# Optimization experiments

Hardware: AMD Instinct MI355X
Metric: run time of the kernel (lower is better)

## Reference

```python
import jax, jax.numpy as jnp
import numpy as np

B, T, D, H = 8, 1024, 512, 8
HD = D // H  # per-head hidden = embed_dim // n_head = 64
EPS = 1e-5


def setup_inputs() -> dict:
    key = jax.random.key(0)
    ks = jax.random.split(key, 8)
    x = jax.random.normal(ks[0], (B, T, D), dtype=jnp.float32)
    sc = 1.0 / np.sqrt(D)
    Wq = jax.random.normal(ks[1], (D, H * HD), dtype=jnp.float32) * sc
    Wk = jax.random.normal(ks[2], (D, H * HD), dtype=jnp.float32) * sc
    Wp = jax.random.normal(ks[3], (H * HD, D), dtype=jnp.float32) * sc
    bq = jnp.zeros((H * HD,), jnp.float32)
    bk = jnp.zeros((H * HD,), jnp.float32)
    bp = jnp.zeros((D,), jnp.float32)
    w_mlp = jax.random.normal(ks[4], (2 * HD,), dtype=jnp.float32) * 0.1
    ln_g = jnp.ones((D,), jnp.float32)
    ln_b = jnp.zeros((D,), jnp.float32)
    return {"x": x, "Wq": Wq, "bq": bq, "Wk": Wk, "bk": bk,
            "Wp": Wp, "bp": bp, "w_mlp": w_mlp, "ln_g": ln_g, "ln_b": ln_b}


def reference(x, Wq, bq, Wk, bk, Wp, bp, w_mlp, ln_g, ln_b):
    b, t, d = x.shape
    h, hd = H, HD
    # q/k projections, split into heads: [B,T,H,hd]
    qx = (x @ Wq + bq).reshape(b, t, h, hd)
    kx = (x @ Wk + bk).reshape(b, t, h, hd)
    # MLP score: tanh(concat(k_j, q_i) . w) == tanh(k_j.w[:hd] + q_i.w[hd:])
    k_s = jnp.einsum('bkhd,d->bkh', kx, w_mlp[:hd])   # [B,K,H]
    q_s = jnp.einsum('bqhd,d->bqh', qx, w_mlp[hd:])   # [B,Q,H]
    score = jnp.tanh(q_s[:, :, None, :] + k_s[:, None, :, :])  # [B,Q,K,H]
    attn = jax.nn.softmax(score, axis=2)  # softmax over k_len
    # values are the key projection kx (bmm(score, kx) in original)
    out = jnp.einsum('bqkh,bkhd->bqhd', attn, kx).reshape(b, t, h * hd)
    out = out @ Wp + bp  # output projection (dropout is identity at eval)
    # residual + LayerNorm
    y = x + out
    mu = jnp.mean(y, axis=-1, keepdims=True)
    var = jnp.var(y, axis=-1, keepdims=True)
    yn = (y - mu) * jax.lax.rsqrt(var + EPS)
    return yn * ln_g + ln_b
```

## Files before the change

### kernel.cpp

```cpp
#include <hip/hip_runtime.h>
#include <cstddef>

#define TT 1024
#define DDIM 512
#define HH 8
#define NND 128
#define NW 72

typedef __attribute__((ext_vector_type(8))) short bfrag;
typedef __attribute__((ext_vector_type(4))) float facc;

#define SC2   2.8853900817779268f
#define L2E   1.4426950408889634f

static __device__ __forceinline__ unsigned bfrne(float f) {
    unsigned u = __float_as_uint(f);
    return (u + 0x7fffu + ((u >> 16) & 1u)) >> 16;
}
static __device__ __forceinline__ unsigned pack2rne(float a, float b) {
    return bfrne(a) | (bfrne(b) << 16);
}
static __device__ __forceinline__ unsigned pack2hu(float a, float b) {
    return ((__float_as_uint(a) + 0x8000u) >> 16) |
           ((__float_as_uint(b) + 0x8000u) & 0xffff0000u);
}
static __device__ __forceinline__ void gl2lds16(const void* g, void* l) {
    __builtin_amdgcn_global_load_lds(
        (const __attribute__((address_space(1))) unsigned int*)g,
        (__attribute__((address_space(3))) unsigned int*)l, 16, 0, 0);
}
static __device__ __forceinline__ float wfun(float z2) {
    float t = __builtin_amdgcn_exp2f(z2);
    float r = __builtin_amdgcn_rcpf(t + 1.f);
    return __builtin_amdgcn_exp2f(fmaf(r, -2.f * L2E, L2E));
}

__global__ __launch_bounds__(256) void prepare_kernel(
    const float* __restrict__ x, const float* __restrict__ Wk,
    const float* __restrict__ Wp, const float* __restrict__ Wq,
    const float* __restrict__ bq, const float* __restrict__ wm,
    unsigned short* __restrict__ xb, unsigned short* __restrict__ WkT,
    unsigned short* __restrict__ WpT, unsigned short* __restrict__ vq2b,
    float* __restrict__ qsb2)
{
    const int bx = blockIdx.x, tid = threadIdx.x;
    if (bx < 2048) {
        const int lane = tid & 63, wave = tid >> 6;
        const int row = bx * 4 + wave;
        const float4* xr = (const float4*)(x + (size_t)row * DDIM);
        float4 x0 = xr[lane * 2], x1 = xr[lane * 2 + 1];
        uint4 st;
        st.x = pack2rne(x0.x, x0.y); st.y = pack2rne(x0.z, x0.w);
        st.z = pack2rne(x1.x, x1.y); st.w = pack2rne(x1.z, x1.w);
        int p = lane ^ (row & 7);
        *(uint4*)(xb + (size_t)row * DDIM + p * 8) = st;
    } else if (bx < 2176) {
        int idx = bx - 2048;
        const float* src = (idx & 64) ? Wp : Wk;
        unsigned short* dst = (idx & 64) ? WpT : WkT;
        idx &= 63;
        const int n0 = (idx & 7) * 64, k0 = (idx >> 3) * 64;
        __shared__ float sT[64][65];
        #pragma unroll
        for (int it = 0; it < 4; ++it) {
            int task = it * 256 + tid;
            int kr = task >> 4, c4 = (task & 15) * 4;
            float4 v = *(const float4*)(src + (size_t)(k0 + kr) * DDIM + n0 + c4);
            sT[kr][c4] = v.x; sT[kr][c4 + 1] = v.y; sT[kr][c4 + 2] = v.z; sT[kr][c4 + 3] = v.w;
        }
        __syncthreads();
        #pragma unroll
        for (int it = 0; it < 2; ++it) {
            int task = it * 256 + tid;
            int n = task >> 3, kg = task & 7;
            unsigned u[4];
            #pragma unroll
            for (int jj = 0; jj < 4; ++jj)
                u[jj] = pack2rne(sT[kg * 8 + jj * 2][n], sT[kg * 8 + jj * 2 + 1][n]);
            int p = ((k0 >> 3) + kg) ^ (n & 7);
            uint4 st; st.x = u[0]; st.y = u[1]; st.z = u[2]; st.w = u[3];
            *(uint4*)(dst + (size_t)(n0 + n) * DDIM + p * 8) = st;
        }
    } else {
        int idx = (bx - 2176) * 256 + tid;
        int h = idx >> 9, d = idx & 511;
        float s = 0.f;
        #pragma unroll 8
        for (int j = 0; j < 64; ++j)
            s = fmaf(Wq[(size_t)d * DDIM + h * 64 + j], wm[64 + j], s);
        vq2b[h * DDIM + d] = (unsigned short)bfrne(s * SC2);
        if (idx < HH) {
            float sb = 0.f;
            for (int j = 0; j < 64; ++j)
                sb = fmaf(bq[idx * 64 + j], wm[64 + j], sb);
            qsb2[idx] = sb * SC2;
        }
    }
}

__global__ __launch_bounds__(256) void gemm1_kernel(
    const unsigned short* __restrict__ A, const unsigned short* __restrict__ B,
    const float* __restrict__ bias, unsigned short* __restrict__ kxTg,
    float* __restrict__ ks2, const float* __restrict__ wm,
    const unsigned short* __restrict__ vq2b, const float* __restrict__ qsb2,
    float* __restrict__ qs2)
{
    __shared__ __align__(16) unsigned short smem[12288];
    unsigned short* sA = smem;
    unsigned short* sB = smem + 8192;
    const int tid = threadIdx.x, lane = tid & 63, wave = tid >> 6;
    const int l15 = lane & 15, quad = lane >> 4;
    const int h = blockIdx.x, row0 = blockIdx.y * 128;
    const int col0 = h * 64;

    facc acc[2][4]; facc accq[2];
    #pragma unroll
    for (int i = 0; i < 2; ++i) {
        #pragma unroll
        for (int j = 0; j < 4; ++j) { acc[i][j][0]=0.f; acc[i][j][1]=0.f; acc[i][j][2]=0.f; acc[i][j][3]=0.f; }
        accq[i][0]=0.f; accq[i][1]=0.f; accq[i][2]=0.f; accq[i][3]=0.f;
    }

    for (int k0 = 0; k0 < 512; k0 += 64) {
        #pragma unroll
        for (int it = 0; it < 4; ++it) {
            int g = it * 256 + tid;
            int r = g >> 3, kg = g & 7;
            gl2lds16(A + (size_t)(row0 + r) * 512 + k0 + kg * 8, &sA[g * 8]);
        }
        #pragma unroll
        for (int it = 0; it < 2; ++it) {
            int g = it * 256 + tid;
            int r = g >> 3, kg = g & 7;
            gl2lds16(B + (size_t)(col0 + r) * 512 + k0 + kg * 8, &sB[g * 8]);
        }
        __syncthreads();
        #pragma unroll
        for (int ks_ = 0; ks_ < 2; ++ks_) {
            int slot = (ks_ * 4 + quad) ^ (l15 & 7);
            bfrag a[2], b[4];
            #pragma unroll
            for (int i = 0; i < 2; ++i)
                a[i] = *(const bfrag*)&sA[(wave * 32 + i * 16 + l15) * 64 + slot * 8];
            #pragma unroll
            for (int nt = 0; nt < 4; ++nt)
                b[nt] = *(const bfrag*)&sB[(nt * 16 + l15) * 64 + slot * 8];
            bfrag bvq = *(const bfrag*)(vq2b + h * 512 + k0 + ks_ * 32 + quad * 8);
            #pragma unroll
            for (int i = 0; i < 2; ++i) {
                #pragma unroll
                for (int nt = 0; nt < 4; ++nt)
                    acc[i][nt] = __builtin_amdgcn_mfma_f32_16x16x32_bf16(a[i], b[nt], acc[i][nt], 0, 0, 0);
                accq[i] = __builtin_amdgcn_mfma_f32_16x16x32_bf16(a[i], bvq, accq[i], 0, 0, 0);
            }
        }
        __syncthreads();
    }

    const int bb = row0 >> 10, t0 = row0 & 1023;
    const float qsbh = qsb2[h];
    float bvv[4], wmv[4];
    #pragma unroll
    for (int nt = 0; nt < 4; ++nt) {
        bvv[nt] = bias[col0 + nt * 16 + l15];
        wmv[nt] = wm[nt * 16 + l15] * SC2;
    }
    float part[2][4];
    #pragma unroll
    for (int i = 0; i < 2; ++i)
        #pragma unroll
        for (int r = 0; r < 4; ++r) part[i][r] = 0.f;

    unsigned short* eT = smem;
    #pragma unroll
    for (int i = 0; i < 2; ++i) {
        int tr = wave * 32 + i * 16 + quad * 4;
        #pragma unroll
        for (int nt = 0; nt < 4; ++nt) {
            int col = nt * 16 + l15;
            float v0 = acc[i][nt][0] + bvv[nt], v1 = acc[i][nt][1] + bvv[nt];
            float v2 = acc[i][nt][2] + bvv[nt], v3 = acc[i][nt][3] + bvv[nt];
            part[i][0] = fmaf(wmv[nt], v0, part[i][0]);
            part[i][1] = fmaf(wmv[nt], v1, part[i][1]);
            part[i][2] = fmaf(wmv[nt], v2, part[i][2]);
            part[i][3] = fmaf(wmv[nt], v3, part[i][3]);
            *(unsigned*)&eT[col * 136 + tr]     = pack2rne(v0, v1);
            *(unsigned*)&eT[col * 136 + tr + 2] = pack2rne(v2, v3);
        }
    }
    #pragma unroll
    for (int i = 0; i < 2; ++i)
        #pragma unroll
        for (int r = 0; r < 4; ++r) {
            float p = part[i][r];
            p += __shfl_xor(p, 1); p += __shfl_xor(p, 2);
            p += __shfl_xor(p, 4); p += __shfl_xor(p, 8);
            if (l15 == 0) {
                size_t o = (size_t)(bb * HH + h) * TT + t0 + wave * 32 + i * 16 + quad * 4 + r;
                ks2[o] = p;
                qs2[o] = accq[i][r] + qsbh;
            }
        }
    __syncthreads();
    unsigned short* kxbase = kxTg + ((size_t)(bb * HH + h) * 64) * TT;
    #pragma unroll
    for (int it = 0; it < 4; ++it) {
        int task = it * 256 + tid;
        int col = task >> 4, seg = task & 15;
        uint4 v = *(const uint4*)&eT[col * 136 + seg * 8];
        int g = (t0 >> 3) + seg;
        int p = g ^ (col & 7);
        *(uint4*)(kxbase + (size_t)col * TT + p * 8) = v;
    }
}

__global__ __launch_bounds__(256) void attn_nodes_kernel(
    const unsigned short* __restrict__ kxTg, const float* __restrict__ qs2,
    const float* __restrict__ ks2, float* __restrict__ node_out,
    float* __restrict__ mn2, float* __restrict__ inv127)
{
    __shared__ __align__(16) unsigned short kxT[64 * 256];
    __shared__ float ksc[1024];
    __shared__ float redl[8];
    const int bh = blockIdx.x;
    const int tid = threadIdx.x, lane = tid & 63, wave = tid >> 6;
    const int l15 = lane & 15, quad = lane >> 4;

    ((float4*)ksc)[tid] = ((const float4*)(ks2 + (size_t)bh * TT))[tid];
    float4 q4 = ((const float4*)(qs2 + (size_t)bh * TT))[tid];
    float mn = fminf(fminf(q4.x, q4.y), fminf(q4.z, q4.w));
    float mx = fmaxf(fmaxf(q4.x, q4.y), fmaxf(q4.z, q4.w));
    #pragma unroll
    for (int off = 32; off > 0; off >>= 1) {
        mn = fminf(mn, __shfl_xor(mn, off));
        mx = fmaxf(mx, __shfl_xor(mx, off));
    }
    if (lane == 0) { redl[wave] = mn; redl[4 + wave] = mx; }
    __syncthreads();
    const float mnv = fminf(fminf(redl[0], redl[1]), fminf(redl[2], redl[3]));
    const float mxv = fmaxf(fmaxf(redl[4], redl[5]), fmaxf(redl[6], redl[7]));
    if (tid == 0) {
        mn2[bh] = mnv;
        inv127[bh] = 127.f / fmaxf(mxv - mnv, 1e-12f);
    }
    const float h2v = (mxv - mnv) * (1.f / 127.f);
    const float zA = mnv + (wave * 16 + l15) * h2v;
    const float zB = zA + 64.f * h2v;

    const unsigned short* kxbase = kxTg + (size_t)bh * 64 * TT;
    facc acc[2][4]; facc accZ[2];
    #pragma unroll
    for (int g = 0; g < 2; ++g) {
        #pragma unroll
        for (int i = 0; i < 4; ++i) { acc[g][i][0]=0.f; acc[g][i][1]=0.f; acc[g][i][2]=0.f; acc[g][i][3]=0.f; }
        accZ[g][0]=0.f; accZ[g][1]=0.f; accZ[g][2]=0.f; accZ[g][3]=0.f;
    }
    bfrag ones;
    #pragma unroll
    for (int j = 0; j < 8; ++j) ones[j] = (short)0x3F80;

    for (int ck = 0; ck < 4; ++ck) {
        #pragma unroll
        for (int it = 0; it < 8; ++it) {
            int g = it * 256 + tid;
            int d = g >> 5, j = g & 31;
            gl2lds16(kxbase + (size_t)d * TT + ck * 256 + j * 8, &kxT[g * 8]);
        }
        __syncthreads();
        #pragma unroll
        for (int kst = 0; kst < 8; ++kst) {
            const float* kvp = &ksc[ck * 256 + kst * 32 + quad * 8];
            float4 kv0 = *(const float4*)kvp;
            float4 kv1 = *(const float4*)(kvp + 4);
            int slot = (kst * 4 + quad) ^ (l15 & 7);
            bfrag bf_[4];
            #pragma unroll
            for (int dt = 0; dt < 4; ++dt)
                bf_[dt] = *(const bfrag*)&kxT[(dt * 16 + l15) * 256 + slot * 8];
            #pragma unroll
            for (int g = 0; g < 2; ++g) {
                float z = g ? zB : zA;
                union { unsigned u[4]; bfrag f; } afu;
                afu.u[0] = pack2hu(wfun(z + kv0.x), wfun(z + kv0.y));
                afu.u[1] = pack2hu(wfun(z + kv0.z), wfun(z + kv0.w));
                afu.u[2] = pack2hu(wfun(z + kv1.x), wfun(z + kv1.y));
                afu.u[3] = pack2hu(wfun(z + kv1.z), wfun(z + kv1.w));
                #pragma unroll
                for (int dt = 0; dt < 4; ++dt)
                    acc[g][dt] = __builtin_amdgcn_mfma_f32_16x16x32_bf16(afu.f, bf_[dt], acc[g][dt], 0, 0, 0);
                accZ[g] = __builtin_amdgcn_mfma_f32_16x16x32_bf16(afu.f, ones, accZ[g], 0, 0, 0);
            }
        }
        __syncthreads();
    }
    float* ob = node_out + (size_t)bh * NND * NW;
    #pragma unroll
    for (int g = 0; g < 2; ++g) {
        #pragma unroll
        for (int r = 0; r < 4; ++r) {
            int node = g * 64 + wave * 16 + quad * 4 + r;
            #pragma unroll
            for (int dt = 0; dt < 4; ++dt)
                ob[(size_t)node * NW + dt * 16 + l15] = acc[g][dt][r];
            if (l15 == 0) ob[(size_t)node * NW + 64] = accZ[g][r];
        }
    }
}

__global__ __launch_bounds__(256) void interp_kernel(
    const float* __restrict__ qs2, const float* __restrict__ node_out,
    const float* __restrict__ mn2, const float* __restrict__ inv127,
    unsigned short* __restrict__ attb)
{
    const int tid = threadIdx.x, lane = tid & 63, wave = tid >> 6;
    const int row = blockIdx.x * 4 + wave;
    const int b = row >> 10, t = row & 1023;
    const int hh2 = lane >> 5, dp = lane & 31;
    #pragma unroll
    for (int h0 = 0; h0 < 8; h0 += 2) {
        const int hh = h0 + hh2;
        const int bh = b * HH + hh;
        float qv = qs2[(size_t)bh * TT + t];
        float u = (qv - mn2[bh]) * inv127[bh];
        int i = (int)floorf(u) - 1;
        i = i < 0 ? 0 : (i > NND - 4 ? NND - 4 : i);
        float s = u - (float)i;
        float s1 = s - 1.f, s2 = s - 2.f, s3 = s - 3.f;
        float w0 = -s1 * s2 * s3 * (1.f / 6.f);
        float w1 = s * s2 * s3 * 0.5f;
        float w2 = -s * s1 * s3 * 0.5f;
        float w3 = s * s1 * s2 * (1.f / 6.f);
        const float* base = node_out + ((size_t)bh * NND + i) * NW;
        float2 v0 = *(const float2*)(base + 2 * dp);
        float2 v1 = *(const float2*)(base + NW + 2 * dp);
        float2 v2 = *(const float2*)(base + 2 * NW + 2 * dp);
        float2 v3 = *(const float2*)(base + 3 * NW + 2 * dp);
        float nx = w0 * v0.x + w1 * v1.x + w2 * v2.x + w3 * v3.x;
        float ny = w0 * v0.y + w1 * v1.y + w2 * v2.y + w3 * v3.y;
        float zz = w0 * base[64] + w1 * base[NW + 64] + w2 * base[2 * NW + 64] + w3 * base[3 * NW + 64];
        float rz = __builtin_amdgcn_rcpf(zz);
        unsigned pk = pack2rne(nx * rz, ny * rz);
        int col = hh * 64 + 2 * dp;
        int p = (col >> 3) ^ (row & 7);
        *(unsigned*)&attb[(size_t)row * DDIM + p * 8 + (col & 7)] = pk;
    }
}

__global__ __launch_bounds__(256) void gemm2_kernel(
    const unsigned short* __restrict__ A, const unsigned short* __restrict__ B,
    const float* __restrict__ bias, const float* __restrict__ x,
    unsigned short* __restrict__ yb)
{
    __shared__ __align__(16) unsigned short smem[12288];
    unsigned short* sA = smem;
    unsigned short* sB = smem + 8192;
    const int tid = threadIdx.x, lane = tid & 63, wave = tid >> 6;
    const int l15 = lane & 15, quad = lane >> 4;
    const int col0 = blockIdx.x * 64, row0 = blockIdx.y * 128;

    facc acc[2][4];
    #pragma unroll
    for (int i = 0; i < 2; ++i)
        #pragma unroll
        for (int j = 0; j < 4; ++j) { acc[i][j][0]=0.f; acc[i][j][1]=0.f; acc[i][j][2]=0.f; acc[i][j][3]=0.f; }

    for (int k0 = 0; k0 < 512; k0 += 64) {
        #pragma unroll
        for (int it = 0; it < 4; ++it) {
            int g = it * 256 + tid;
            int r = g >> 3, kg = g & 7;
            gl2lds16(A + (size_t)(row0 + r) * 512 + k0 + kg * 8, &sA[g * 8]);
        }
        #pragma unroll
        for (int it = 0; it < 2; ++it) {
            int g = it * 256 + tid;
            int r = g >> 3, kg = g & 7;
            gl2lds16(B + (size_t)(col0 + r) * 512 + k0 + kg * 8, &sB[g * 8]);
        }
        __syncthreads();
        #pragma unroll
        for (int ks_ = 0; ks_ < 2; ++ks_) {
            int slot = (ks_ * 4 + quad) ^ (l15 & 7);
            bfrag a[2], b[4];
            #pragma unroll
            for (int i = 0; i < 2; ++i)
                a[i] = *(const bfrag*)&sA[(wave * 32 + i * 16 + l15) * 64 + slot * 8];
            #pragma unroll
            for (int nt = 0; nt < 4; ++nt)
                b[nt] = *(const bfrag*)&sB[(nt * 16 + l15) * 64 + slot * 8];
            #pragma unroll
            for (int i = 0; i < 2; ++i)
                #pragma unroll
                for (int nt = 0; nt < 4; ++nt)
                    acc[i][nt] = __builtin_amdgcn_mfma_f32_16x16x32_bf16(a[i], b[nt], acc[i][nt], 0, 0, 0);
        }
        __syncthreads();
    }
    float bvv[4];
    #pragma unroll
    for (int nt = 0; nt < 4; ++nt) bvv[nt] = bias[col0 + nt * 16 + l15];
    unsigned short* yT = smem;
    #pragma unroll
    for (int i = 0; i < 2; ++i) {
        #pragma unroll
        for (int nt = 0; nt < 4; ++nt) {
            int col = nt * 16 + l15;
            #pragma unroll
            for (int r = 0; r < 4; ++r) {
                int row = wave * 32 + i * 16 + quad * 4 + r;
                float xv = x[(size_t)(row0 + row) * DDIM + col0 + col];
                float y = acc[i][nt][r] + bvv[nt] + xv;
                yT[row * 72 + col] = (unsigned short)bfrne(y);
            }
        }
    }
    __syncthreads();
    #pragma unroll
    for (int it = 0; it < 4; ++it) {
        int task = it * 256 + tid;
        int row = task >> 3, seg = task & 7;
        uint4 v = *(const uint4*)&yT[row * 72 + seg * 8];
        *(uint4*)(yb + (size_t)(row0 + row) * DDIM + col0 + seg * 8) = v;
    }
}

__global__ __launch_bounds__(256) void ln_kernel(
    const unsigned short* __restrict__ yb, const float* __restrict__ g,
    const float* __restrict__ bet, float* __restrict__ out)
{
    const int tid = threadIdx.x, lane = tid & 63, wave = tid >> 6;
    const int row = blockIdx.x * 4 + wave;
    uint4 v = *(const uint4*)(yb + (size_t)row * DDIM + lane * 8);
    float y[8];
    y[0] = __uint_as_float(v.x << 16); y[1] = __uint_as_float(v.x & 0xffff0000u);
    y[2] = __uint_as_float(v.y << 16); y[3] = __uint_as_float(v.y & 0xffff0000u);
    y[4] = __uint_as_float(v.z << 16); y[5] = __uint_as_float(v.z & 0xffff0000u);
    y[6] = __uint_as_float(v.w << 16); y[7] = __uint_as_float(v.w & 0xffff0000u);
    float s = 0.f, s2 = 0.f;
    #pragma unroll
    for (int i = 0; i < 8; ++i) { s += y[i]; s2 = fmaf(y[i], y[i], s2); }
    #pragma unroll
    for (int off = 32; off > 0; off >>= 1) {
        s += __shfl_xor(s, off);
        s2 += __shfl_xor(s2, off);
    }
    float mu = s * (1.f / 512.f);
    float var = s2 * (1.f / 512.f) - mu * mu;
    float inv = rsqrtf(var + 1e-5f);
    const float4* gp = (const float4*)(g + lane * 8);
    const float4* bp = (const float4*)(bet + lane * 8);
    float4 g0 = gp[0], g1 = gp[1], b0 = bp[0], b1 = bp[1];
    float4 o0, o1;
    o0.x = (y[0] - mu) * inv * g0.x + b0.x; o0.y = (y[1] - mu) * inv * g0.y + b0.y;
    o0.z = (y[2] - mu) * inv * g0.z + b0.z; o0.w = (y[3] - mu) * inv * g0.w + b0.w;
    o1.x = (y[4] - mu) * inv * g1.x + b1.x; o1.y = (y[5] - mu) * inv * g1.y + b1.y;
    o1.z = (y[6] - mu) * inv * g1.z + b1.z; o1.w = (y[7] - mu) * inv * g1.w + b1.w;
    float4* op = (float4*)(out + (size_t)row * DDIM);
    op[lane * 2] = o0; op[lane * 2 + 1] = o1;
}

extern "C" void kernel_launch(void* const* d_in, const int* in_sizes, int n_in,
                              void* d_out, int out_size, void* d_ws, size_t ws_size,
                              hipStream_t stream)
{
    const float* x    = (const float*)d_in[0];
    const float* Wq   = (const float*)d_in[1];
    const float* bq   = (const float*)d_in[2];
    const float* Wk   = (const float*)d_in[3];
    const float* bk   = (const float*)d_in[4];
    const float* Wp   = (const float*)d_in[5];
    const float* bp   = (const float*)d_in[6];
    const float* wm   = (const float*)d_in[7];
    const float* ln_g = (const float*)d_in[8];
    const float* ln_b = (const float*)d_in[9];
    float* out = (float*)d_out;

    float* ws = (float*)d_ws;
    float*          qsb2 = ws;
    unsigned short* vq2b = (unsigned short*)(ws + 64);
    unsigned short* WkT  = (unsigned short*)(ws + 2112);
    unsigned short* WpT  = (unsigned short*)(ws + 133184);
    unsigned short* xb   = (unsigned short*)(ws + 264256);
    unsigned short* kxTg = (unsigned short*)(ws + 2361408);
    float*          qs2  = ws + 4458560;
    float*          ks2  = ws + 4524096;
    unsigned short* attb = (unsigned short*)(ws + 4589632);
    float*          ndo  = ws + 6686784;
    float*          mn2  = ws + 7276608;
    float*          i127 = ws + 7276672;
    unsigned short* yb   = xb;

    prepare_kernel<<<2192, 256, 0, stream>>>(x, Wk, Wp, Wq, bq, wm,
                                             xb, WkT, WpT, vq2b, qsb2);
    gemm1_kernel<<<dim3(8, 64), 256, 0, stream>>>(xb, WkT, bk, kxTg, ks2, wm,
                                                  vq2b, qsb2, qs2);
    attn_nodes_kernel<<<64, 256, 0, stream>>>(kxTg, qs2, ks2, ndo, mn2, i127);
    interp_kernel<<<2048, 256, 0, stream>>>(qs2, ndo, mn2, i127, attb);
    gemm2_kernel<<<dim3(8, 64), 256, 0, stream>>>(attb, WpT, bp, x, yb);
    ln_kernel<<<2048, 256, 0, stream>>>(yb, ln_g, ln_b, out);
}
```

Before: 151.4 us.

## Fuse all six stages into one cooperative persistent kernel with grid syncs

Replaces the six separate kernel launches with a single cooperative mega-kernel of 256 persistent blocks. Stages are separated by grid.sync() and work is distributed by grid-stride loops. The attention-node stage now splits each batch-head's key range across two blocks that write partial sums, and the interpolation stage adds the two halves. This removes launch gaps and inter-kernel drains, but leaves only one 256-thread block per CU, which cuts occupancy in the GEMM and elementwise stages and adds grid-barrier costs.

```diff
diff --git a/kernel.cpp b/kernel.cpp
--- a/kernel.cpp
+++ b/kernel.cpp
@@ -1,5 +1,8 @@
 #include <hip/hip_runtime.h>
+#include <hip/hip_cooperative_groups.h>
 #include <cstddef>
+
+namespace cg = cooperative_groups;
 
 #define TT 1024
 #define DDIM 512
@@ -35,428 +38,411 @@
     return __builtin_amdgcn_exp2f(fmaf(r, -2.f * L2E, L2E));
 }
 
-__global__ __launch_bounds__(256) void prepare_kernel(
-    const float* __restrict__ x, const float* __restrict__ Wk,
-    const float* __restrict__ Wp, const float* __restrict__ Wq,
-    const float* __restrict__ bq, const float* __restrict__ wm,
+union SMem {
+    float sT[64][65];
+    unsigned short g1[12288];
+    struct { unsigned short kxT[64 * 256]; float ksc[1024]; float redl[8]; } at;
+};
+
+__global__ __launch_bounds__(256, 1) void mega_kernel(
+    const float* __restrict__ x, const float* __restrict__ Wq,
+    const float* __restrict__ bq, const float* __restrict__ Wk,
+    const float* __restrict__ bk, const float* __restrict__ Wp,
+    const float* __restrict__ bp, const float* __restrict__ wm,
+    const float* __restrict__ ln_g, const float* __restrict__ ln_b,
+    float* __restrict__ out,
     unsigned short* __restrict__ xb, unsigned short* __restrict__ WkT,
     unsigned short* __restrict__ WpT, unsigned short* __restrict__ vq2b,
-    float* __restrict__ qsb2)
+    float* __restrict__ qsb2, unsigned short* __restrict__ kxTg,
+    float* __restrict__ qs2, float* __restrict__ ks2,
+    float* __restrict__ ndo, float* __restrict__ mn2,
+    float* __restrict__ i127, unsigned short* __restrict__ attb,
+    unsigned short* __restrict__ yb)
 {
-    const int bx = blockIdx.x, tid = threadIdx.x;
-    if (bx < 2048) {
-        const int lane = tid & 63, wave = tid >> 6;
-        const int row = bx * 4 + wave;
-        const float4* xr = (const float4*)(x + (size_t)row * DDIM);
-        float4 x0 = xr[lane * 2], x1 = xr[lane * 2 + 1];
-        uint4 st;
-        st.x = pack2rne(x0.x, x0.y); st.y = pack2rne(x0.z, x0.w);
-        st.z = pack2rne(x1.x, x1.y); st.w = pack2rne(x1.z, x1.w);
-        int p = lane ^ (row & 7);
-        *(uint4*)(xb + (size_t)row * DDIM + p * 8) = st;
-    } else if (bx < 2176) {
-        int idx = bx - 2048;
-        const float* src = (idx & 64) ? Wp : Wk;
-        unsigned short* dst = (idx & 64) ? WpT : WkT;
-        idx &= 63;
-        const int n0 = (idx & 7) * 64, k0 = (idx >> 3) * 64;
-        __shared__ float sT[64][65];
+    __shared__ SMem sm;
+    cg::grid_group grid = cg::this_grid();
+    const int bid = blockIdx.x, tid = threadIdx.x;
+    const int lane = tid & 63, wave = tid >> 6;
+    const int l15 = lane & 15, quad = lane >> 4;
+
+    for (int t = bid; t < 2192; t += 256) {
+        if (t < 2048) {
+            const int row = t * 4 + wave;
+            const float4* xr = (const float4*)(x + (size_t)row * DDIM);
+            float4 x0 = xr[lane * 2], x1 = xr[lane * 2 + 1];
+            uint4 st;
+            st.x = pack2rne(x0.x, x0.y); st.y = pack2rne(x0.z, x0.w);
+            st.z = pack2rne(x1.x, x1.y); st.w = pack2rne(x1.z, x1.w);
+            int p = lane ^ (row & 7);
+            *(uint4*)(xb + (size_t)row * DDIM + p * 8) = st;
+        } else if (t < 2176) {
+            int idx = t - 2048;
+            const float* src = (idx & 64) ? Wp : Wk;
+            unsigned short* dst = (idx & 64) ? WpT : WkT;
+            idx &= 63;
+            const int n0 = (idx & 7) * 64, k0 = (idx >> 3) * 64;
+            #pragma unroll
+            for (int it = 0; it < 4; ++it) {
+                int task = it * 256 + tid;
+                int kr = task >> 4, c4 = (task & 15) * 4;
+                float4 v = *(const float4*)(src + (size_t)(k0 + kr) * DDIM + n0 + c4);
+                sm.sT[kr][c4] = v.x; sm.sT[kr][c4 + 1] = v.y;
+                sm.sT[kr][c4 + 2] = v.z; sm.sT[kr][c4 + 3] = v.w;
+            }
+            __syncthreads();
+            #pragma unroll
+            for (int it = 0; it < 2; ++it) {
+                int task = it * 256 + tid;
+                int n = task >> 3, kg = task & 7;
+                unsigned u[4];
+                #pragma unroll
+                for (int jj = 0; jj < 4; ++jj)
+                    u[jj] = pack2rne(sm.sT[kg * 8 + jj * 2][n], sm.sT[kg * 8 + jj * 2 + 1][n]);
+                int p = ((k0 >> 3) + kg) ^ (n & 7);
+                uint4 st; st.x = u[0]; st.y = u[1]; st.z = u[2]; st.w = u[3];
+                *(uint4*)(dst + (size_t)(n0 + n) * DDIM + p * 8) = st;
+            }
+            __syncthreads();
+        } else {
+            int idx = (t - 2176) * 256 + tid;
+            int h = idx >> 9, d = idx & 511;
+            float s = 0.f;
+            #pragma unroll 8
+            for (int j = 0; j < 64; ++j)
+                s = fmaf(Wq[(size_t)d * DDIM + h * 64 + j], wm[64 + j], s);
+            vq2b[h * DDIM + d] = (unsigned short)bfrne(s * SC2);
+            if (idx < HH) {
+                float sb = 0.f;
+                for (int j = 0; j < 64; ++j)
+                    sb = fmaf(bq[idx * 64 + j], wm[64 + j], sb);
+                qsb2[idx] = sb * SC2;
+            }
+        }
+    }
+    grid.sync();
+
+    for (int t = bid; t < 512; t += 256) {
+        const int h = t & 7, row0 = (t >> 3) * 128;
+        const int col0 = h * 64;
+        unsigned short* sA = sm.g1;
+        unsigned short* sB = sm.g1 + 8192;
+
+        facc acc[2][4]; facc accq[2];
+        #pragma unroll
+        for (int i = 0; i < 2; ++i) {
+            #pragma unroll
+            for (int j = 0; j < 4; ++j) { acc[i][j][0]=0.f; acc[i][j][1]=0.f; acc[i][j][2]=0.f; acc[i][j][3]=0.f; }
+            accq[i][0]=0.f; accq[i][1]=0.f; accq[i][2]=0.f; accq[i][3]=0.f;
+        }
+        for (int k0 = 0; k0 < 512; k0 += 64) {
+            #pragma unroll
+            for (int it = 0; it < 4; ++it) {
+                int g = it * 256 + tid;
+                int r = g >> 3, kg = g & 7;
+                gl2lds16(xb + (size_t)(row0 + r) * 512 + k0 + kg * 8, &sA[g * 8]);
+            }
+            #pragma unroll
+            for (int it = 0; it < 2; ++it) {
+                int g = it * 256 + tid;
+                int r = g >> 3, kg = g & 7;
+                gl2lds16(WkT + (size_t)(col0 + r) * 512 + k0 + kg * 8, &sB[g * 8]);
+            }
+            __syncthreads();
+            #pragma unroll
+            for (int ks_ = 0; ks_ < 2; ++ks_) {
+                int slot = (ks_ * 4 + quad) ^ (l15 & 7);
+                bfrag a[2], b[4];
+                #pragma unroll
+                for (int i = 0; i < 2; ++i)
+                    a[i] = *(const bfrag*)&sA[(wave * 32 + i * 16 + l15) * 64 + slot * 8];
+                #pragma unroll
+                for (int nt = 0; nt < 4; ++nt)
+                    b[nt] = *(const bfrag*)&sB[(nt * 16 + l15) * 64 + slot * 8];
+                bfrag bvq = *(const bfrag*)(vq2b + h * 512 + k0 + ks_ * 32 + quad * 8);
+                #pragma unroll
+                for (int i = 0; i < 2; ++i) {
+                    #pragma unroll
+                    for (int nt = 0; nt < 4; ++nt)
+                        acc[i][nt] = __builtin_amdgcn_mfma_f32_16x16x32_bf16(a[i], b[nt], acc[i][nt], 0, 0, 0);
+                    accq[i] = __builtin_amdgcn_mfma_f32_16x16x32_bf16(a[i], bvq, accq[i], 0, 0, 0);
+                }
+            }
+            __syncthreads();
+        }
+        const int bb = row0 >> 10, t0 = row0 & 1023;
+        const float qsbh = qsb2[h];
+        float bvv[4], wmv[4];
+        #pragma unroll
+        for (int nt = 0; nt < 4; ++nt) {
+            bvv[nt] = bk[col0 + nt * 16 + l15];
+            wmv[nt] = wm[nt * 16 + l15] * SC2;
+        }
+        float part[2][4];
+        #pragma unroll
+        for (int i = 0; i < 2; ++i)
+            #pragma unroll
+            for (int r = 0; r < 4; ++r) part[i][r] = 0.f;
+        unsigned short* eT = sm.g1;
+        #pragma unroll
+        for (int i = 0; i < 2; ++i) {
+            int tr = wave * 32 + i * 16 + quad * 4;
+            #pragma unroll
+            for (int nt = 0; nt < 4; ++nt) {
+                int col = nt * 16 + l15;
+                float v0 = acc[i][nt][0] + bvv[nt], v1 = acc[i][nt][1] + bvv[nt];
+                float v2 = acc[i][nt][2] + bvv[nt], v3 = acc[i][nt][3] + bvv[nt];
+                part[i][0] = fmaf(wmv[nt], v0, part[i][0]);
+                part[i][1] = fmaf(wmv[nt], v1, part[i][1]);
+                part[i][2] = fmaf(wmv[nt], v2, part[i][2]);
+                part[i][3] = fmaf(wmv[nt], v3, part[i][3]);
+                *(unsigned*)&eT[col * 136 + tr]     = pack2rne(v0, v1);
+                *(unsigned*)&eT[col * 136 + tr + 2] = pack2rne(v2, v3);
+            }
+        }
+        #pragma unroll
+        for (int i = 0; i < 2; ++i)
+            #pragma unroll
+            for (int r = 0; r < 4; ++r) {
+                float p = part[i][r];
+                p += __shfl_xor(p, 1); p += __shfl_xor(p, 2);
+                p += __shfl_xor(p, 4); p += __shfl_xor(p, 8);
+                if (l15 == 0) {
+                    size_t o = (size_t)(bb * HH + h) * TT + t0 + wave * 32 + i * 16 + quad * 4 + r;
+                    ks2[o] = p;
+                    qs2[o] = accq[i][r] + qsbh;
+                }
+            }
+        __syncthreads();
+        unsigned short* kxbase = kxTg + ((size_t)(bb * HH + h) * 64) * TT;
         #pragma unroll
         for (int it = 0; it < 4; ++it) {
             int task = it * 256 + tid;
-            int kr = task >> 4, c4 = (task & 15) * 4;
-            float4 v = *(const float4*)(src + (size_t)(k0 + kr) * DDIM + n0 + c4);
-            sT[kr][c4] = v.x; sT[kr][c4 + 1] = v.y; sT[kr][c4 + 2] = v.z; sT[kr][c4 + 3] = v.w;
+            int col = task >> 4, seg = task & 15;
+            uint4 v = *(const uint4*)&eT[col * 136 + seg * 8];
+            int g = (t0 >> 3) + seg;
+            int p = g ^ (col & 7);
+            *(uint4*)(kxbase + (size_t)col * TT + p * 8) = v;
         }
         __syncthreads();
-        #pragma unroll
-        for (int it = 0; it < 2; ++it) {
+    }
+    grid.sync();
+
+    {
+        const int t = bid;
+        const int bh = t >> 2, nh = (t >> 1) & 1, ckh = t & 1;
+        ((float4*)sm.at.ksc)[tid] = ((const float4*)(ks2 + (size_t)bh * TT))[tid];
+        float4 q4 = ((const float4*)(qs2 + (size_t)bh * TT))[tid];
+        float mn = fminf(fminf(q4.x, q4.y), fminf(q4.z, q4.w));
+        float mx = fmaxf(fmaxf(q4.x, q4.y), fmaxf(q4.z, q4.w));
+        #pragma unroll
+        for (int off = 32; off > 0; off >>= 1) {
+            mn = fminf(mn, __shfl_xor(mn, off));
+            mx = fmaxf(mx, __shfl_xor(mx, off));
+        }
+        if (lane == 0) { sm.at.redl[wave] = mn; sm.at.redl[4 + wave] = mx; }
+        __syncthreads();
+        const float mnv = fminf(fminf(sm.at.redl[0], sm.at.redl[1]), fminf(sm.at.redl[2], sm.at.redl[3]));
+        const float mxv = fmaxf(fmaxf(sm.at.redl[4], sm.at.redl[5]), fmaxf(sm.at.redl[6], sm.at.redl[7]));
+        if (tid == 0 && nh == 0 && ckh == 0) {
+            mn2[bh] = mnv;
+            i127[bh] = 127.f / fmaxf(mxv - mnv, 1e-12f);
+        }
+        const float h2v = (mxv - mnv) * (1.f / 127.f);
+        const float zA = mnv + (nh * 64 + wave * 16 + l15) * h2v;
+
+        const unsigned short* kxbase = kxTg + (size_t)bh * 64 * TT;
+        facc acc[4]; facc accZ;
+        #pragma unroll
+        for (int i = 0; i < 4; ++i) { acc[i][0]=0.f; acc[i][1]=0.f; acc[i][2]=0.f; acc[i][3]=0.f; }
+        accZ[0]=0.f; accZ[1]=0.f; accZ[2]=0.f; accZ[3]=0.f;
+        bfrag ones;
+        #pragma unroll
+        for (int j = 0; j < 8; ++j) ones[j] = (short)0x3F80;
+
+        #pragma unroll
+        for (int cc = 0; cc < 2; ++cc) {
+            const int ck = ckh * 2 + cc;
+            #pragma unroll
+            for (int it = 0; it < 8; ++it) {
+                int g = it * 256 + tid;
+                int d = g >> 5, j = g & 31;
+                gl2lds16(kxbase + (size_t)d * TT + ck * 256 + j * 8, &sm.at.kxT[g * 8]);
+            }
+            __syncthreads();
+            #pragma unroll
+            for (int kst = 0; kst < 8; ++kst) {
+                const float* kvp = &sm.at.ksc[ck * 256 + kst * 32 + quad * 8];
+                float4 kv0 = *(const float4*)kvp;
+                float4 kv1 = *(const float4*)(kvp + 4);
+                int slot = (kst * 4 + quad) ^ (l15 & 7);
+                union { unsigned u[4]; bfrag f; } afu;
+                afu.u[0] = pack2hu(wfun(zA + kv0.x), wfun(zA + kv0.y));
+                afu.u[1] = pack2hu(wfun(zA + kv0.z), wfun(zA + kv0.w));
+                afu.u[2] = pack2hu(wfun(zA + kv1.x), wfun(zA + kv1.y));
+                afu.u[3] = pack2hu(wfun(zA + kv1.z), wfun(zA + kv1.w));
+                #pragma unroll
+                for (int dt = 0; dt < 4; ++dt) {
+                    bfrag bf_ = *(const bfrag*)&sm.at.kxT[(dt * 16 + l15) * 256 + slot * 8];
+                    acc[dt] = __builtin_amdgcn_mfma_f32_16x16x32_bf16(afu.f, bf_, acc[dt], 0, 0, 0);
+                }
+                accZ = __builtin_amdgcn_mfma_f32_16x16x32_bf16(afu.f, ones, accZ, 0, 0, 0);
+            }
+            __syncthreads();
+        }
+        float* ob = ndo + ((size_t)(ckh * 64 + bh) * NND) * NW;
+        #pragma unroll
+        for (int r = 0; r < 4; ++r) {
+            int node = nh * 64 + wave * 16 + quad * 4 + r;
+            #pragma unroll
+            for (int dt = 0; dt < 4; ++dt)
+                ob[(size_t)node * NW + dt * 16 + l15] = acc[dt][r];
+            if (l15 == 0) ob[(size_t)node * NW + 64] = accZ[r];
+        }
+    }
+    grid.sync();
+
+    for (int t = bid; t < 2048; t += 256) {
+        const int row = t * 4 + wave;
+        const int b = row >> 10, tt = row & 1023;
+        const int hh2 = lane >> 5, dp = lane & 31;
+        #pragma unroll
+        for (int h0 = 0; h0 < 8; h0 += 2) {
+            const int hh = h0 + hh2;
+            const int bh = b * HH + hh;
+            float qv = qs2[(size_t)bh * TT + tt];
+            float u = (qv - mn2[bh]) * i127[bh];
+            int i = (int)floorf(u) - 1;
+            i = i < 0 ? 0 : (i > NND - 4 ? NND - 4 : i);
+            float s = u - (float)i;
+            float s1 = s - 1.f, s2 = s - 2.f, s3 = s - 3.f;
+            float w0 = -s1 * s2 * s3 * (1.f / 6.f);
+            float w1 = s * s2 * s3 * 0.5f;
+            float w2 = -s * s1 * s3 * 0.5f;
+            float w3 = s * s1 * s2 * (1.f / 6.f);
+            const float* b0p = ndo + ((size_t)bh * NND + i) * NW;
+            const float* b1p = ndo + ((size_t)(64 + bh) * NND + i) * NW;
+            float nx = 0.f, ny = 0.f, zz = 0.f;
+            #pragma unroll
+            for (int c = 0; c < 2; ++c) {
+                const float* base = c ? b1p : b0p;
+                float2 v0 = *(const float2*)(base + 2 * dp);
+                float2 v1 = *(const float2*)(base + NW + 2 * dp);
+                float2 v2 = *(const float2*)(base + 2 * NW + 2 * dp);
+                float2 v3 = *(const float2*)(base + 3 * NW + 2 * dp);
+                nx += w0 * v0.x + w1 * v1.x + w2 * v2.x + w3 * v3.x;
+                ny += w0 * v0.y + w1 * v1.y + w2 * v2.y + w3 * v3.y;
+                zz += w0 * base[64] + w1 * base[NW + 64] + w2 * base[2 * NW + 64] + w3 * base[3 * NW + 64];
+            }
+            float rz = __builtin_amdgcn_rcpf(zz);
+            unsigned pk = pack2rne(nx * rz, ny * rz);
+            int col = hh * 64 + 2 * dp;
+            int p = (col >> 3) ^ (row & 7);
+            *(unsigned*)&attb[(size_t)row * DDIM + p * 8 + (col & 7)] = pk;
+        }
+    }
+    grid.sync();
+
+    for (int t = bid; t < 512; t += 256) {
+        const int col0 = (t & 7) * 64, row0 = (t >> 3) * 128;
+        unsigned short* sA = sm.g1;
+        unsigned short* sB = sm.g1 + 8192;
+        facc acc[2][4];
+        #pragma unroll
+        for (int i = 0; i < 2; ++i)
+            #pragma unroll
+            for (int j = 0; j < 4; ++j) { acc[i][j][0]=0.f; acc[i][j][1]=0.f; acc[i][j][2]=0.f; acc[i][j][3]=0.f; }
+        for (int k0 = 0; k0 < 512; k0 += 64) {
+            #pragma unroll
+            for (int it = 0; it < 4; ++it) {
+                int g = it * 256 + tid;
+                int r = g >> 3, kg = g & 7;
+                gl2lds16(attb + (size_t)(row0 + r) * 512 + k0 + kg * 8, &sA[g * 8]);
+            }
+            #pragma unroll
+            for (int it = 0; it < 2; ++it) {
+                int g = it * 256 + tid;
+                int r = g >> 3, kg = g & 7;
+                gl2lds16(WpT + (size_t)(col0 + r) * 512 + k0 + kg * 8, &sB[g * 8]);
+            }
+            __syncthreads();
+            #pragma unroll
+            for (int ks_ = 0; ks_ < 2; ++ks_) {
+                int slot = (ks_ * 4 + quad) ^ (l15 & 7);
+                bfrag a[2], b[4];
+                #pragma unroll
+                for (int i = 0; i < 2; ++i)
+                    a[i] = *(const bfrag*)&sA[(wave * 32 + i * 16 + l15) * 64 + slot * 8];
+                #pragma unroll
+                for (int nt = 0; nt < 4; ++nt)
+                    b[nt] = *(const bfrag*)&sB[(nt * 16 + l15) * 64 + slot * 8];
+                #pragma unroll
+                for (int i = 0; i < 2; ++i)
+                    #pragma unroll
+                    for (int nt = 0; nt < 4; ++nt)
+                        acc[i][nt] = __builtin_amdgcn_mfma_f32_16x16x32_bf16(a[i], b[nt], acc[i][nt], 0, 0, 0);
+            }
+            __syncthreads();
+        }
+        float bvv[4];
+        #pragma unroll
+        for (int nt = 0; nt < 4; ++nt) bvv[nt] = bp[col0 + nt * 16 + l15];
+        unsigned short* yT = sm.g1;
+        #pragma unroll
+        for (int i = 0; i < 2; ++i) {
+            #pragma unroll
+            for (int nt = 0; nt < 4; ++nt) {
+                int col = nt * 16 + l15;
+                #pragma unroll
+                for (int r = 0; r < 4; ++r) {
+                    int row = wave * 32 + i * 16 + quad * 4 + r;
+                    float xv = x[(size_t)(row0 + row) * DDIM + col0 + col];
+                    float y = acc[i][nt][r] + bvv[nt] + xv;
+                    yT[row * 72 + col] = (unsigned short)bfrne(y);
+                }
+            }
+        }
+        __syncthreads();
+        #pragma unroll
+        for (int it = 0; it < 4; ++it) {
             int task = it * 256 + tid;
-            int n = task >> 3, kg = task & 7;
-            unsigned u[4];
-            #pragma unroll
-            for (int jj = 0; jj < 4; ++jj)
-                u[jj] = pack2rne(sT[kg * 8 + jj * 2][n], sT[kg * 8 + jj * 2 + 1][n]);
-            int p = ((k0 >> 3) + kg) ^ (n & 7);
-            uint4 st; st.x = u[0]; st.y = u[1]; st.z = u[2]; st.w = u[3];
-            *(uint4*)(dst + (size_t)(n0 + n) * DDIM + p * 8) = st;
-        }
-    } else {
-        int idx = (bx - 2176) * 256 + tid;
-        int h = idx >> 9, d = idx & 511;
-        float s = 0.f;
-        #pragma unroll 8
-        for (int j = 0; j < 64; ++j)
-            s = fmaf(Wq[(size_t)d * DDIM + h * 64 + j], wm[64 + j], s);
-        vq2b[h * DDIM + d] = (unsigned short)bfrne(s * SC2);
-        if (idx < HH) {
-            float sb = 0.f;
-            for (int j = 0; j < 64; ++j)
-                sb = fmaf(bq[idx * 64 + j], wm[64 + j], sb);
-            qsb2[idx] = sb * SC2;
-        }
-    }
-}
-
-__global__ __launch_bounds__(256) void gemm1_kernel(
-    const unsigned short* __restrict__ A, const unsigned short* __restrict__ B,
-    const float* __restrict__ bias, unsigned short* __restrict__ kxTg,
-    float* __restrict__ ks2, const float* __restrict__ wm,
-    const unsigned short* __restrict__ vq2b, const float* __restrict__ qsb2,
-    float* __restrict__ qs2)
-{
-    __shared__ __align__(16) unsigned short smem[12288];
-    unsigned short* sA = smem;
-    unsigned short* sB = smem + 8192;
-    const int tid = threadIdx.x, lane = tid & 63, wave = tid >> 6;
-    const int l15 = lane & 15, quad = lane >> 4;
-    const int h = blockIdx.x, row0 = blockIdx.y * 128;
-    const int col0 = h * 64;
-
-    facc acc[2][4]; facc accq[2];
-    #pragma unroll
-    for (int i = 0; i < 2; ++i) {
-        #pragma unroll
-        for (int j = 0; j < 4; ++j) { acc[i][j][0]=0.f; acc[i][j][1]=0.f; acc[i][j][2]=0.f; acc[i][j][3]=0.f; }
-        accq[i][0]=0.f; accq[i][1]=0.f; accq[i][2]=0.f; accq[i][3]=0.f;
-    }
-
-    for (int k0 = 0; k0 < 512; k0 += 64) {
-        #pragma unroll
-        for (int it = 0; it < 4; ++it) {
-            int g = it * 256 + tid;
-            int r = g >> 3, kg = g & 7;
-            gl2lds16(A + (size_t)(row0 + r) * 512 + k0 + kg * 8, &sA[g * 8]);
-        }
-        #pragma unroll
-        for (int it = 0; it < 2; ++it) {
-            int g = it * 256 + tid;
-            int r = g >> 3, kg = g & 7;
-            gl2lds16(B + (size_t)(col0 + r) * 512 + k0 + kg * 8, &sB[g * 8]);
+            int row = task >> 3, seg = task & 7;
+            uint4 v = *(const uint4*)&yT[row * 72 + seg * 8];
+            *(uint4*)(yb + (size_t)(row0 + row) * DDIM + col0 + seg * 8) = v;
         }
         __syncthreads();
-        #pragma unroll
-        for (int ks_ = 0; ks_ < 2; ++ks_) {
-            int slot = (ks_ * 4 + quad) ^ (l15 & 7);
-            bfrag a[2], b[4];
-            #pragma unroll
-            for (int i = 0; i < 2; ++i)
-                a[i] = *(const bfrag*)&sA[(wave * 32 + i * 16 + l15) * 64 + slot * 8];
-            #pragma unroll
-            for (int nt = 0; nt < 4; ++nt)
-                b[nt] = *(const bfrag*)&sB[(nt * 16 + l15) * 64 + slot * 8];
-            bfrag bvq = *(const bfrag*)(vq2b + h * 512 + k0 + ks_ * 32 + quad * 8);
-            #pragma unroll
-            for (int i = 0; i < 2; ++i) {
-                #pragma unroll
-                for (int nt = 0; nt < 4; ++nt)
-                    acc[i][nt] = __builtin_amdgcn_mfma_f32_16x16x32_bf16(a[i], b[nt], acc[i][nt], 0, 0, 0);
-                accq[i] = __builtin_amdgcn_mfma_f32_16x16x32_bf16(a[i], bvq, accq[i], 0, 0, 0);
-            }
-        }
-        __syncthreads();
-    }
-
-    const int bb = row0 >> 10, t0 = row0 & 1023;
-    const float qsbh = qsb2[h];
-    float bvv[4], wmv[4];
-    #pragma unroll
-    for (int nt = 0; nt < 4; ++nt) {
-        bvv[nt] = bias[col0 + nt * 16 + l15];
-        wmv[nt] = wm[nt * 16 + l15] * SC2;
-    }
-    float part[2][4];
-    #pragma unroll
-    for (int i = 0; i < 2; ++i)
-        #pragma unroll
-        for (int r = 0; r < 4; ++r) part[i][r] = 0.f;
-
-    unsigned short* eT = smem;
-    #pragma unroll
-    for (int i = 0; i < 2; ++i) {
-        int tr = wave * 32 + i * 16 + quad * 4;
-        #pragma unroll
-        for (int nt = 0; nt < 4; ++nt) {
-            int col = nt * 16 + l15;
-            float v0 = acc[i][nt][0] + bvv[nt], v1 = acc[i][nt][1] + bvv[nt];
-            float v2 = acc[i][nt][2] + bvv[nt], v3 = acc[i][nt][3] + bvv[nt];
-            part[i][0] = fmaf(wmv[nt], v0, part[i][0]);
-            part[i][1] = fmaf(wmv[nt], v1, part[i][1]);
-            part[i][2] = fmaf(wmv[nt], v2, part[i][2]);
-            part[i][3] = fmaf(wmv[nt], v3, part[i][3]);
-            *(unsigned*)&eT[col * 136 + tr]     = pack2rne(v0, v1);
-            *(unsigned*)&eT[col * 136 + tr + 2] = pack2rne(v2, v3);
-        }
-    }
-    #pragma unroll
-    for (int i = 0; i < 2; ++i)
-        #pragma unroll
-        for (int r = 0; r < 4; ++r) {
-            float p = part[i][r];
-            p += __shfl_xor(p, 1); p += __shfl_xor(p, 2);
-            p += __shfl_xor(p, 4); p += __shfl_xor(p, 8);
-            if (l15 == 0) {
-                size_t o = (size_t)(bb * HH + h) * TT + t0 + wave * 32 + i * 16 + quad * 4 + r;
-                ks2[o] = p;
-                qs2[o] = accq[i][r] + qsbh;
-            }
-        }
-    __syncthreads();
-    unsigned short* kxbase = kxTg + ((size_t)(bb * HH + h) * 64) * TT;
-    #pragma unroll
-    for (int it = 0; it < 4; ++it) {
-        int task = it * 256 + tid;
-        int col = task >> 4, seg = task & 15;
-        uint4 v = *(const uint4*)&eT[col * 136 + seg * 8];
-        int g = (t0 >> 3) + seg;
-        int p = g ^ (col & 7);
-        *(uint4*)(kxbase + (size_t)col * TT + p * 8) = v;
-    }
-}
-
-__global__ __launch_bounds__(256) void attn_nodes_kernel(
-    const unsigned short* __restrict__ kxTg, const float* __restrict__ qs2,
-    const float* __restrict__ ks2, float* __restrict__ node_out,
-    float* __restrict__ mn2, float* __restrict__ inv127)
-{
-    __shared__ __align__(16) unsigned short kxT[64 * 256];
-    __shared__ float ksc[1024];
-    __shared__ float redl[8];
-    const int bh = blockIdx.x;
-    const int tid = threadIdx.x, lane = tid & 63, wave = tid >> 6;
-    const int l15 = lane & 15, quad = lane >> 4;
-
-    ((float4*)ksc)[tid] = ((const float4*)(ks2 + (size_t)bh * TT))[tid];
-    float4 q4 = ((const float4*)(qs2 + (size_t)bh * TT))[tid];
-    float mn = fminf(fminf(q4.x, q4.y), fminf(q4.z, q4.w));
-    float mx = fmaxf(fmaxf(q4.x, q4.y), fmaxf(q4.z, q4.w));
-    #pragma unroll
-    for (int off = 32; off > 0; off >>= 1) {
-        mn = fminf(mn, __shfl_xor(mn, off));
-        mx = fmaxf(mx, __shfl_xor(mx, off));
-    }
-    if (lane == 0) { redl[wave] = mn; redl[4 + wave] = mx; }
-    __syncthreads();
-    const float mnv = fminf(fminf(redl[0], redl[1]), fminf(redl[2], redl[3]));
-    const float mxv = fmaxf(fmaxf(redl[4], redl[5]), fmaxf(redl[6], redl[7]));
-    if (tid == 0) {
-        mn2[bh] = mnv;
-        inv127[bh] = 127.f / fmaxf(mxv - mnv, 1e-12f);
-    }
-    const float h2v = (mxv - mnv) * (1.f / 127.f);
-    const float zA = mnv + (wave * 16 + l15) * h2v;
-    const float zB = zA + 64.f * h2v;
-
-    const unsigned short* kxbase = kxTg + (size_t)bh * 64 * TT;
-    facc acc[2][4]; facc accZ[2];
-    #pragma unroll
-    for (int g = 0; g < 2; ++g) {
-        #pragma unroll
-        for (int i = 0; i < 4; ++i) { acc[g][i][0]=0.f; acc[g][i][1]=0.f; acc[g][i][2]=0.f; acc[g][i][3]=0.f; }
-        accZ[g][0]=0.f; accZ[g][1]=0.f; accZ[g][2]=0.f; accZ[g][3]=0.f;
-    }
-    bfrag ones;
-    #pragma unroll
-    for (int j = 0; j < 8; ++j) ones[j] = (short)0x3F80;
-
-    for (int ck = 0; ck < 4; ++ck) {
-        #pragma unroll
-        for (int it = 0; it < 8; ++it) {
-            int g = it * 256 + tid;
-            int d = g >> 5, j = g & 31;
-            gl2lds16(kxbase + (size_t)d * TT + ck * 256 + j * 8, &kxT[g * 8]);
-        }
-        __syncthreads();
-        #pragma unroll
-        for (int kst = 0; kst < 8; ++kst) {
-            const float* kvp = &ksc[ck * 256 + kst * 32 + quad * 8];
-            float4 kv0 = *(const float4*)kvp;
-            float4 kv1 = *(const float4*)(kvp + 4);
-            int slot = (kst * 4 + quad) ^ (l15 & 7);
-            bfrag bf_[4];
-            #pragma unroll
-            for (int dt = 0; dt < 4; ++dt)
-                bf_[dt] = *(const bfrag*)&kxT[(dt * 16 + l15) * 256 + slot * 8];
-            #pragma unroll
-            for (int g = 0; g < 2; ++g) {
-                float z = g ? zB : zA;
-                union { unsigned u[4]; bfrag f; } afu;
-                afu.u[0] = pack2hu(wfun(z + kv0.x), wfun(z + kv0.y));
-                afu.u[1] = pack2hu(wfun(z + kv0.z), wfun(z + kv0.w));
-                afu.u[2] = pack2hu(wfun(z + kv1.x), wfun(z + kv1.y));
-                afu.u[3] = pack2hu(wfun(z + kv1.z), wfun(z + kv1.w));
-                #pragma unroll
-                for (int dt = 0; dt < 4; ++dt)
-                    acc[g][dt] = __builtin_amdgcn_mfma_f32_16x16x32_bf16(afu.f, bf_[dt], acc[g][dt], 0, 0, 0);
-                accZ[g] = __builtin_amdgcn_mfma_f32_16x16x32_bf16(afu.f, ones, accZ[g], 0, 0, 0);
-            }
-        }
-        __syncthreads();
-    }
-    float* ob = node_out + (size_t)bh * NND * NW;
-    #pragma unroll
-    for (int g = 0; g < 2; ++g) {
-        #pragma unroll
-        for (int r = 0; r < 4; ++r) {
-            int node = g * 64 + wave * 16 + quad * 4 + r;
-            #pragma unroll
-            for (int dt = 0; dt < 4; ++dt)
-                ob[(size_t)node * NW + dt * 16 + l15] = acc[g][dt][r];
-            if (l15 == 0) ob[(size_t)node * NW + 64] = accZ[g][r];
-        }
-    }
-}
-
-__global__ __launch_bounds__(256) void interp_kernel(
-    const float* __restrict__ qs2, const float* __restrict__ node_out,
-    const float* __restrict__ mn2, const float* __restrict__ inv127,
-    unsigned short* __restrict__ attb)
-{
-    const int tid = threadIdx.x, lane = tid & 63, wave = tid >> 6;
-    const int row = blockIdx.x * 4 + wave;
-    const int b = row >> 10, t = row & 1023;
-    const int hh2 = lane >> 5, dp = lane & 31;
-    #pragma unroll
-    for (int h0 = 0; h0 < 8; h0 += 2) {
-        const int hh = h0 + hh2;
-        const int bh = b * HH + hh;
-        float qv = qs2[(size_t)bh * TT + t];
-        float u = (qv - mn2[bh]) * inv127[bh];
-        int i = (int)floorf(u) - 1;
-        i = i < 0 ? 0 : (i > NND - 4 ? NND - 4 : i);
-        float s = u - (float)i;
-        float s1 = s - 1.f, s2 = s - 2.f, s3 = s - 3.f;
-        float w0 = -s1 * s2 * s3 * (1.f / 6.f);
-        float w1 = s * s2 * s3 * 0.5f;
-        float w2 = -s * s1 * s3 * 0.5f;
-        float w3 = s * s1 * s2 * (1.f / 6.f);
-        const float* base = node_out + ((size_t)bh * NND + i) * NW;
-        float2 v0 = *(const float2*)(base + 2 * dp);
-        float2 v1 = *(const float2*)(base + NW + 2 * dp);
-        float2 v2 = *(const float2*)(base + 2 * NW + 2 * dp);
-        float2 v3 = *(const float2*)(base + 3 * NW + 2 * dp);
-        float nx = w0 * v0.x + w1 * v1.x + w2 * v2.x + w3 * v3.x;
-        float ny = w0 * v0.y + w1 * v1.y + w2 * v2.y + w3 * v3.y;
-        float zz = w0 * base[64] + w1 * base[NW + 64] + w2 * base[2 * NW + 64] + w3 * base[3 * NW + 64];
-        float rz = __builtin_amdgcn_rcpf(zz);
-        unsigned pk = pack2rne(nx * rz, ny * rz);
-        int col = hh * 64 + 2 * dp;
-        int p = (col >> 3) ^ (row & 7);
-        *(unsigned*)&attb[(size_t)row * DDIM + p * 8 + (col & 7)] = pk;
-    }
-}
-
-__global__ __launch_bounds__(256) void gemm2_kernel(
-    const unsigned short* __restrict__ A, const unsigned short* __restrict__ B,
-    const float* __restrict__ bias, const float* __restrict__ x,
-    unsigned short* __restrict__ yb)
-{
-    __shared__ __align__(16) unsigned short smem[12288];
-    unsigned short* sA = smem;
-    unsigned short* sB = smem + 8192;
-    const int tid = threadIdx.x, lane = tid & 63, wave = tid >> 6;
-    const int l15 = lane & 15, quad = lane >> 4;
-    const int col0 = blockIdx.x * 64, row0 = blockIdx.y * 128;
-
-    facc acc[2][4];
-    #pragma unroll
-    for (int i = 0; i < 2; ++i)
-        #pragma unroll
-        for (int j = 0; j < 4; ++j) { acc[i][j][0]=0.f; acc[i][j][1]=0.f; acc[i][j][2]=0.f; acc[i][j][3]=0.f; }
-
-    for (int k0 = 0; k0 < 512; k0 += 64) {
-        #pragma unroll
-        for (int it = 0; it < 4; ++it) {
-            int g = it * 256 + tid;
-            int r = g >> 3, kg = g & 7;
-            gl2lds16(A + (size_t)(row0 + r) * 512 + k0 + kg * 8, &sA[g * 8]);
-        }
-        #pragma unroll
-        for (int it = 0; it < 2; ++it) {
-            int g = it * 256 + tid;
-            int r = g >> 3, kg = g & 7;
-            gl2lds16(B + (size_t)(col0 + r) * 512 + k0 + kg * 8, &sB[g * 8]);
-        }
-        __syncthreads();
-        #pragma unroll
-        for (int ks_ = 0; ks_ < 2; ++ks_) {
-            int slot = (ks_ * 4 + quad) ^ (l15 & 7);
-            bfrag a[2], b[4];
-            #pragma unroll
-            for (int i = 0; i < 2; ++i)
-                a[i] = *(const bfrag*)&sA[(wave * 32 + i * 16 + l15) * 64 + slot * 8];
-            #pragma unroll
-            for (int nt = 0; nt < 4; ++nt)
-                b[nt] = *(const bfrag*)&sB[(nt * 16 + l15) * 64 + slot * 8];
-            #pragma unroll
-            for (int i = 0; i < 2; ++i)
-                #pragma unroll
-                for (int nt = 0; nt < 4; ++nt)
-                    acc[i][nt] = __builtin_amdgcn_mfma_f32_16x16x32_bf16(a[i], b[nt], acc[i][nt], 0, 0, 0);
-        }
-        __syncthreads();
-    }
-    float bvv[4];
-    #pragma unroll
-    for (int nt = 0; nt < 4; ++nt) bvv[nt] = bias[col0 + nt * 16 + l15];
-    unsigned short* yT = smem;
-    #pragma unroll
-    for (int i = 0; i < 2; ++i) {
-        #pragma unroll
-        for (int nt = 0; nt < 4; ++nt) {
-            int col = nt * 16 + l15;
-            #pragma unroll
-            for (int r = 0; r < 4; ++r) {
-                int row = wave * 32 + i * 16 + quad * 4 + r;
-                float xv = x[(size_t)(row0 + row) * DDIM + col0 + col];
-                float y = acc[i][nt][r] + bvv[nt] + xv;
-                yT[row * 72 + col] = (unsigned short)bfrne(y);
-            }
-        }
-    }
-    __syncthreads();
-    #pragma unroll
-    for (int it = 0; it < 4; ++it) {
-        int task = it * 256 + tid;
-        int row = task >> 3, seg = task & 7;
-        uint4 v = *(const uint4*)&yT[row * 72 + seg * 8];
-        *(uint4*)(yb + (size_t)(row0 + row) * DDIM + col0 + seg * 8) = v;
-    }
-}
-
-__global__ __launch_bounds__(256) void ln_kernel(
-    const unsigned short* __restrict__ yb, const float* __restrict__ g,
-    const float* __restrict__ bet, float* __restrict__ out)
-{
-    const int tid = threadIdx.x, lane = tid & 63, wave = tid >> 6;
-    const int row = blockIdx.x * 4 + wave;
-    uint4 v = *(const uint4*)(yb + (size_t)row * DDIM + lane * 8);
-    float y[8];
-    y[0] = __uint_as_float(v.x << 16); y[1] = __uint_as_float(v.x & 0xffff0000u);
-    y[2] = __uint_as_float(v.y << 16); y[3] = __uint_as_float(v.y & 0xffff0000u);
-    y[4] = __uint_as_float(v.z << 16); y[5] = __uint_as_float(v.z & 0xffff0000u);
-    y[6] = __uint_as_float(v.w << 16); y[7] = __uint_as_float(v.w & 0xffff0000u);
-    float s = 0.f, s2 = 0.f;
-    #pragma unroll
-    for (int i = 0; i < 8; ++i) { s += y[i]; s2 = fmaf(y[i], y[i], s2); }
-    #pragma unroll
-    for (int off = 32; off > 0; off >>= 1) {
-        s += __shfl_xor(s, off);
-        s2 += __shfl_xor(s2, off);
-    }
-    float mu = s * (1.f / 512.f);
-    float var = s2 * (1.f / 512.f) - mu * mu;
-    float inv = rsqrtf(var + 1e-5f);
-    const float4* gp = (const float4*)(g + lane * 8);
-    const float4* bp = (const float4*)(bet + lane * 8);
-    float4 g0 = gp[0], g1 = gp[1], b0 = bp[0], b1 = bp[1];
-    float4 o0, o1;
-    o0.x = (y[0] - mu) * inv * g0.x + b0.x; o0.y = (y[1] - mu) * inv * g0.y + b0.y;
-    o0.z = (y[2] - mu) * inv * g0.z + b0.z; o0.w = (y[3] - mu) * inv * g0.w + b0.w;
-    o1.x = (y[4] - mu) * inv * g1.x + b1.x; o1.y = (y[5] - mu) * inv * g1.y + b1.y;
-    o1.z = (y[6] - mu) * inv * g1.z + b1.z; o1.w = (y[7] - mu) * inv * g1.w + b1.w;
-    float4* op = (float4*)(out + (size_t)row * DDIM);
-    op[lane * 2] = o0; op[lane * 2 + 1] = o1;
+    }
+    grid.sync();
+
+    for (int t = bid; t < 2048; t += 256) {
+        const int row = t * 4 + wave;
+        uint4 v = *(const uint4*)(yb + (size_t)row * DDIM + lane * 8);
+        float y[8];
+        y[0] = __uint_as_float(v.x << 16); y[1] = __uint_as_float(v.x & 0xffff0000u);
+        y[2] = __uint_as_float(v.y << 16); y[3] = __uint_as_float(v.y & 0xffff0000u);
+        y[4] = __uint_as_float(v.z << 16); y[5] = __uint_as_float(v.z & 0xffff0000u);
+        y[6] = __uint_as_float(v.w << 16); y[7] = __uint_as_float(v.w & 0xffff0000u);
+        float s = 0.f, s2 = 0.f;
+        #pragma unroll
+        for (int i = 0; i < 8; ++i) { s += y[i]; s2 = fmaf(y[i], y[i], s2); }
+        #pragma unroll
+        for (int off = 32; off > 0; off >>= 1) {
+            s += __shfl_xor(s, off);
+            s2 += __shfl_xor(s2, off);
+        }
+        float mu = s * (1.f / 512.f);
+        float var = s2 * (1.f / 512.f) - mu * mu;
+        float inv = rsqrtf(var + 1e-5f);
+        const float4* gp = (const float4*)(ln_g + lane * 8);
+        const float4* bpt = (const float4*)(ln_b + lane * 8);
+        float4 g0 = gp[0], g1 = gp[1], b0 = bpt[0], b1 = bpt[1];
+        float4 o0, o1;
+        o0.x = (y[0] - mu) * inv * g0.x + b0.x; o0.y = (y[1] - mu) * inv * g0.y + b0.y;
+        o0.z = (y[2] - mu) * inv * g0.z + b0.z; o0.w = (y[3] - mu) * inv * g0.w + b0.w;
+        o1.x = (y[4] - mu) * inv * g1.x + b1.x; o1.y = (y[5] - mu) * inv * g1.y + b1.y;
+        o1.z = (y[6] - mu) * inv * g1.z + b1.z; o1.w = (y[7] - mu) * inv * g1.w + b1.w;
+        float4* op = (float4*)(out + (size_t)row * DDIM);
+        op[lane * 2] = o0; op[lane * 2 + 1] = o1;
+    }
 }
 
 extern "C" void kernel_launch(void* const* d_in, const int* in_sizes, int n_in,
@@ -486,16 +472,17 @@
     float*          ks2  = ws + 4524096;
     unsigned short* attb = (unsigned short*)(ws + 4589632);
     float*          ndo  = ws + 6686784;
-    float*          mn2  = ws + 7276608;
-    float*          i127 = ws + 7276672;
+    float*          mn2  = ws + 7866432;
+    float*          i127 = ws + 7866496;
     unsigned short* yb   = xb;
 
-    prepare_kernel<<<2192, 256, 0, stream>>>(x, Wk, Wp, Wq, bq, wm,
-                                             xb, WkT, WpT, vq2b, qsb2);
-    gemm1_kernel<<<dim3(8, 64), 256, 0, stream>>>(xb, WkT, bk, kxTg, ks2, wm,
-                                                  vq2b, qsb2, qs2);
-    attn_nodes_kernel<<<64, 256, 0, stream>>>(kxTg, qs2, ks2, ndo, mn2, i127);
-    interp_kernel<<<2048, 256, 0, stream>>>(qs2, ndo, mn2, i127, attb);
-    gemm2_kernel<<<dim3(8, 64), 256, 0, stream>>>(attb, WpT, bp, x, yb);
-    ln_kernel<<<2048, 256, 0, stream>>>(yb, ln_g, ln_b, out);
-}
+    void* args[] = {
+        (void*)&x, (void*)&Wq, (void*)&bq, (void*)&Wk, (void*)&bk,
+        (void*)&Wp, (void*)&bp, (void*)&wm, (void*)&ln_g, (void*)&ln_b,
+        (void*)&out, (void*)&xb, (void*)&WkT, (void*)&WpT, (void*)&vq2b,
+        (void*)&qsb2, (void*)&kxTg, (void*)&qs2, (void*)&ks2, (void*)&ndo,
+        (void*)&mn2, (void*)&i127, (void*)&attb, (void*)&yb
+    };
+    hipLaunchCooperativeKernel((void*)mega_kernel, dim3(256), dim3(256),
+                               args, 0, stream);
+}
```

Measured after the change: 343.0 us. 2.27x slower.
